# Performance work log

Measured on AMD Instinct MI355X. Metric: run time of the kernel, lower is better.

Reference implementation:

```python
import jax, jax.numpy as jnp
import numpy as np

N, M = 32768, 1024

def setup_inputs() -> dict:
    key = jax.random.key(0)
    k1, k2, k3, k4, k5 = jax.random.split(key, 5)
    origins = jax.random.normal(k1, (N, 2), dtype=jnp.float32)
    directions = jax.random.normal(k2, (N, 2), dtype=jnp.float32)
    means = jax.random.normal(k3, (M, 4), dtype=jnp.float32)
    # SPD covariances: A @ A^T + I so the inverse is well-defined
    A = jax.random.normal(k4, (M, 4, 4), dtype=jnp.float32) * 0.5
    covariances = jnp.einsum('mij,mkj->mik', A, A) + jnp.eye(4, dtype=jnp.float32)
    labels_embedding = jax.random.normal(k5, (M,), dtype=jnp.float32)
    return {"origins": origins, "directions": directions, "means": means,
            "covariances": covariances, "labels_embedding": labels_embedding}

def reference(origins, directions, means, covariances, labels_embedding):
    pos = jnp.concatenate([origins, directions], axis=1)          # [N,4]
    Sigma_inv = jnp.linalg.inv(covariances)                       # [M,4,4]
    diffs = pos[:, None, :] - means[None, :, :]                   # [N,M,4]
    quad = jnp.einsum('nmd,mde,nme->nm', diffs, Sigma_inv, diffs)  # [N,M]
    pdf = jnp.exp(-0.5 * quad) * labels_embedding[None, :]        # [N,M]
    prob = jax.nn.sigmoid(jnp.sum(pdf, axis=1))                   # [N]
    return prob.reshape(-1, 1)
```

## Files before the change

kernel.cpp:

```cpp
#include <hip/hip_runtime.h>
#include <math.h>

#define M_GAUSS 1024
#define N_RAYS  32768

typedef float v2f __attribute__((ext_vector_type(2)));

__device__ __forceinline__ float fexp2(float x) {
#if __has_builtin(__builtin_amdgcn_exp2f)
    return __builtin_amdgcn_exp2f(x);
#else
    return exp2f(x);
#endif
}

__device__ __forceinline__ v2f fma2(v2f a, v2f b, v2f c) {
#if __has_builtin(__builtin_elementwise_fma)
    return __builtin_elementwise_fma(a, b, c);
#else
    v2f r; r.x = fmaf(a.x, b.x, c.x); r.y = fmaf(a.y, b.y, c.y); return r;
#endif
}

__device__ __forceinline__ v2f mkv2(float x, float y) { v2f r; r.x = x; r.y = y; return r; }

__global__ __launch_bounds__(1024, 8) void decoder_fused(
    const float2* __restrict__ org,
    const float2* __restrict__ dir,
    const float*  __restrict__ means,
    const float*  __restrict__ covs,
    const float*  __restrict__ labels,
    float*        __restrict__ out)
{
    __shared__ float smemW[M_GAUSS * 16];

    const int tid  = threadIdx.x;
    const int lane = tid & 63;
    const int wave = tid >> 6;
    const int ray  = (blockIdx.x << 6) + lane;

    {
        const int g = tid;
        const float4* C4 = reinterpret_cast<const float4*>(covs + 16 * g);
        const float4 r0 = C4[0], r1 = C4[1], r2 = C4[2], r3 = C4[3];
        const float a00=r0.x, a01=r0.y, a02=r0.z, a03=r0.w;
        const float a10=r1.x, a11=r1.y, a12=r1.z, a13=r1.w;
        const float a20=r2.x, a21=r2.y, a22=r2.z, a23=r2.w;
        const float a30=r3.x, a31=r3.y, a32=r3.z, a33=r3.w;

        const float s0=a00*a11-a01*a10, s1=a00*a12-a02*a10, s2=a00*a13-a03*a10;
        const float s3=a01*a12-a02*a11, s4=a01*a13-a03*a11, s5=a02*a13-a03*a12;
        const float c5=a22*a33-a23*a32, c4=a21*a33-a23*a31, c3=a21*a32-a22*a31;
        const float c2=a20*a33-a23*a30, c1=a20*a32-a22*a30, c0=a20*a31-a21*a30;
        const float det = s0*c5 - s1*c4 + s2*c3 + s3*c2 - s4*c1 + s5*c0;
        const float id  = 1.0f / det;

        const float b00=( a11*c5 - a12*c4 + a13*c3)*id;
        const float b01=(-a01*c5 + a02*c4 - a03*c3)*id;
        const float b10=(-a10*c5 + a12*c2 - a13*c1)*id;
        const float b11=( a00*c5 - a02*c2 + a03*c1)*id;
        const float b20=( a10*c4 - a11*c2 + a13*c0)*id;
        const float b21=(-a00*c4 + a01*c2 - a03*c0)*id;
        const float b30=(-a10*c3 + a11*c1 - a12*c0)*id;
        const float b31=( a00*c3 - a01*c1 + a02*c0)*id;
        const float b02=( a31*s5 - a32*s4 + a33*s3)*id;
        const float b03=(-a21*s5 + a22*s4 - a23*s3)*id;
        const float b12=(-a30*s5 + a32*s2 - a33*s1)*id;
        const float b13=( a20*s5 - a22*s2 + a23*s1)*id;
        const float b22=( a30*s4 - a31*s2 + a33*s0)*id;
        const float b23=(-a20*s4 + a21*s2 - a23*s0)*id;
        const float b32=(-a30*s3 + a31*s1 - a32*s0)*id;
        const float b33=( a20*s3 - a21*s1 + a22*s0)*id;

        const float m01=0.5f*(b01+b10), m02=0.5f*(b02+b20), m03=0.5f*(b03+b30);
        const float m12=0.5f*(b12+b21), m13=0.5f*(b13+b31), m23=0.5f*(b23+b32);

        const float4 mu = reinterpret_cast<const float4*>(means)[g];
        const float u0=mu.x, u1=mu.y, u2=mu.z, u3=mu.w;
        const float v0 = b00*u0 + m01*u1 + m02*u2 + m03*u3;
        const float v1 = m01*u0 + b11*u1 + m12*u2 + m13*u3;
        const float v2 = m02*u0 + m12*u1 + b22*u2 + m23*u3;
        const float v3 = m03*u0 + m13*u1 + m23*u2 + b33*u3;
        const float cc = u0*v0 + u1*v1 + u2*v2 + u3*v3;

        const float k  = -0.72134752044448170368f;
        const float k2 = 2.0f * k;
        float* w = smemW + 16 * g;
        w[0]  = k*b00;   w[1]  = k*b11;   w[2]  = k*b22;   w[3]  = k*b33;
        w[4]  = k2*m01;  w[5]  = k2*m02;  w[6]  = k2*m03;  w[7]  = k2*m12;
        w[8]  = k2*m13;  w[9]  = k2*m23;  w[10] = -k2*v0;  w[11] = -k2*v1;
        w[12] = -k2*v2;  w[13] = -k2*v3;  w[14] = k*cc;    w[15] = labels[g];
    }
    __syncthreads();

    const float2 o = org[ray];
    const float2 d = dir[ray];
    const float p0=o.x, p1=o.y, p2=d.x, p3=d.y;

    const v2f f0 = mkv2(p0*p0, p1*p1);
    const v2f f1 = mkv2(p2*p2, p3*p3);
    const v2f f2 = mkv2(p0*p1, p0*p2);
    const v2f f3 = mkv2(p0*p3, p1*p2);
    const v2f f4 = mkv2(p1*p3, p2*p3);
    const v2f f5 = mkv2(p0, p1);
    const v2f f6 = mkv2(p2, p3);

    float acc = 0.0f;
    const int mBase = wave << 6;

    #pragma unroll 4
    for (int m = 0; m < 64; ++m) {
        const float4* w4 = reinterpret_cast<const float4*>(smemW + ((mBase + m) << 4));
        const float4 wa = w4[0];
        const float4 wb = w4[1];
        const float4 wc = w4[2];
        const float4 wd = w4[3];

        v2f cA = mkv2(wa.x, wa.y) * f0;
        v2f cB = mkv2(wa.z, wa.w) * f1;
        cA = fma2(mkv2(wb.x, wb.y), f2, cA);
        cB = fma2(mkv2(wb.z, wb.w), f3, cB);
        cA = fma2(mkv2(wc.x, wc.y), f4, cA);
        cB = fma2(mkv2(wc.z, wc.w), f5, cB);
        cA = fma2(mkv2(wd.x, wd.y), f6, cA);
        cA = cA + cB;
        const float s = (cA.x + cA.y) + wd.z;
        acc = fmaf(wd.w, fexp2(s), acc);
    }

    __syncthreads();
    smemW[(wave << 6) + lane] = acc;
    __syncthreads();

    if (wave == 0) {
        float t = 0.0f;
        #pragma unroll
        for (int w = 0; w < 16; ++w) t += smemW[(w << 6) + lane];
        const float e = fexp2(-t * 1.4426950408889634f);
        out[ray] = 1.0f / (1.0f + e);
    }
}

extern "C" void kernel_launch(void* const* d_in, const int* in_sizes, int n_in,
                              void* d_out, int out_size, void* d_ws, size_t ws_size,
                              hipStream_t stream) {
    const float* origins    = (const float*)d_in[0];
    const float* directions = (const float*)d_in[1];
    const float* means      = (const float*)d_in[2];
    const float* covs       = (const float*)d_in[3];
    const float* labels     = (const float*)d_in[4];
    float* out = (float*)d_out;

    decoder_fused<<<dim3(N_RAYS / 64), dim3(1024), 0, stream>>>(
        (const float2*)origins, (const float2*)directions, means, covs, labels, out);
}
```

Measured before the change: 80.76 us.

## Split covariance-inverse prep into a separate kernel and read weights from global memory

```diff
diff --git a/kernel.cpp b/kernel.cpp
--- a/kernel.cpp
+++ b/kernel.cpp
@@ -24,74 +24,76 @@
 
 __device__ __forceinline__ v2f mkv2(float x, float y) { v2f r; r.x = x; r.y = y; return r; }
 
-__global__ __launch_bounds__(1024, 8) void decoder_fused(
+__global__ __launch_bounds__(256) void prep_kernel(
+    const float* __restrict__ means,
+    const float* __restrict__ covs,
+    const float* __restrict__ labels,
+    float* __restrict__ W)
+{
+    const int g = blockIdx.x * blockDim.x + threadIdx.x;
+    if (g >= M_GAUSS) return;
+
+    const float4* C4 = reinterpret_cast<const float4*>(covs + 16 * g);
+    const float4 r0 = C4[0], r1 = C4[1], r2 = C4[2], r3 = C4[3];
+    const float a00=r0.x, a01=r0.y, a02=r0.z, a03=r0.w;
+    const float a10=r1.x, a11=r1.y, a12=r1.z, a13=r1.w;
+    const float a20=r2.x, a21=r2.y, a22=r2.z, a23=r2.w;
+    const float a30=r3.x, a31=r3.y, a32=r3.z, a33=r3.w;
+
+    const float s0=a00*a11-a01*a10, s1=a00*a12-a02*a10, s2=a00*a13-a03*a10;
+    const float s3=a01*a12-a02*a11, s4=a01*a13-a03*a11, s5=a02*a13-a03*a12;
+    const float c5=a22*a33-a23*a32, c4=a21*a33-a23*a31, c3=a21*a32-a22*a31;
+    const float c2=a20*a33-a23*a30, c1=a20*a32-a22*a30, c0=a20*a31-a21*a30;
+    const float det = s0*c5 - s1*c4 + s2*c3 + s3*c2 - s4*c1 + s5*c0;
+    const float id  = 1.0f / det;
+
+    const float b00=( a11*c5 - a12*c4 + a13*c3)*id;
+    const float b01=(-a01*c5 + a02*c4 - a03*c3)*id;
+    const float b10=(-a10*c5 + a12*c2 - a13*c1)*id;
+    const float b11=( a00*c5 - a02*c2 + a03*c1)*id;
+    const float b20=( a10*c4 - a11*c2 + a13*c0)*id;
+    const float b21=(-a00*c4 + a01*c2 - a03*c0)*id;
+    const float b30=(-a10*c3 + a11*c1 - a12*c0)*id;
+    const float b31=( a00*c3 - a01*c1 + a02*c0)*id;
+    const float b02=( a31*s5 - a32*s4 + a33*s3)*id;
+    const float b03=(-a21*s5 + a22*s4 - a23*s3)*id;
+    const float b12=(-a30*s5 + a32*s2 - a33*s1)*id;
+    const float b13=( a20*s5 - a22*s2 + a23*s1)*id;
+    const float b22=( a30*s4 - a31*s2 + a33*s0)*id;
+    const float b23=(-a20*s4 + a21*s2 - a23*s0)*id;
+    const float b32=(-a30*s3 + a31*s1 - a32*s0)*id;
+    const float b33=( a20*s3 - a21*s1 + a22*s0)*id;
+
+    const float m01=0.5f*(b01+b10), m02=0.5f*(b02+b20), m03=0.5f*(b03+b30);
+    const float m12=0.5f*(b12+b21), m13=0.5f*(b13+b31), m23=0.5f*(b23+b32);
+
+    const float4 mu = reinterpret_cast<const float4*>(means)[g];
+    const float u0=mu.x, u1=mu.y, u2=mu.z, u3=mu.w;
+    const float v0 = b00*u0 + m01*u1 + m02*u2 + m03*u3;
+    const float v1 = m01*u0 + b11*u1 + m12*u2 + m13*u3;
+    const float v2 = m02*u0 + m12*u1 + b22*u2 + m23*u3;
+    const float v3 = m03*u0 + m13*u1 + m23*u2 + b33*u3;
+    const float cc = u0*v0 + u1*v1 + u2*v2 + u3*v3;
+
+    const float k  = -0.72134752044448170368f;
+    const float k2 = 2.0f * k;
+    float4* w4 = reinterpret_cast<float4*>(W + 16 * g);
+    w4[0] = make_float4(k*b00,  k*b11,  k*b22,  k*b33);
+    w4[1] = make_float4(k2*m01, k2*m02, k2*m03, k2*m12);
+    w4[2] = make_float4(k2*m13, k2*m23, -k2*v0, -k2*v1);
+    w4[3] = make_float4(-k2*v2, -k2*v3, k*cc,   labels[g]);
+}
+
+__global__ __launch_bounds__(1024, 8) void decoder_kernel(
     const float2* __restrict__ org,
     const float2* __restrict__ dir,
-    const float*  __restrict__ means,
-    const float*  __restrict__ covs,
-    const float*  __restrict__ labels,
+    const float*  __restrict__ W,
     float*        __restrict__ out)
 {
-    __shared__ float smemW[M_GAUSS * 16];
-
     const int tid  = threadIdx.x;
     const int lane = tid & 63;
     const int wave = tid >> 6;
     const int ray  = (blockIdx.x << 6) + lane;
-
-    {
-        const int g = tid;
-        const float4* C4 = reinterpret_cast<const float4*>(covs + 16 * g);
-        const float4 r0 = C4[0], r1 = C4[1], r2 = C4[2], r3 = C4[3];
-        const float a00=r0.x, a01=r0.y, a02=r0.z, a03=r0.w;
-        const float a10=r1.x, a11=r1.y, a12=r1.z, a13=r1.w;
-        const float a20=r2.x, a21=r2.y, a22=r2.z, a23=r2.w;
-        const float a30=r3.x, a31=r3.y, a32=r3.z, a33=r3.w;
-
-        const float s0=a00*a11-a01*a10, s1=a00*a12-a02*a10, s2=a00*a13-a03*a10;
-        const float s3=a01*a12-a02*a11, s4=a01*a13-a03*a11, s5=a02*a13-a03*a12;
-        const float c5=a22*a33-a23*a32, c4=a21*a33-a23*a31, c3=a21*a32-a22*a31;
-        const float c2=a20*a33-a23*a30, c1=a20*a32-a22*a30, c0=a20*a31-a21*a30;
-        const float det = s0*c5 - s1*c4 + s2*c3 + s3*c2 - s4*c1 + s5*c0;
-        const float id  = 1.0f / det;
-
-        const float b00=( a11*c5 - a12*c4 + a13*c3)*id;
-        const float b01=(-a01*c5 + a02*c4 - a03*c3)*id;
-        const float b10=(-a10*c5 + a12*c2 - a13*c1)*id;
-        const float b11=( a00*c5 - a02*c2 + a03*c1)*id;
-        const float b20=( a10*c4 - a11*c2 + a13*c0)*id;
-        const float b21=(-a00*c4 + a01*c2 - a03*c0)*id;
-        const float b30=(-a10*c3 + a11*c1 - a12*c0)*id;
-        const float b31=( a00*c3 - a01*c1 + a02*c0)*id;
-        const float b02=( a31*s5 - a32*s4 + a33*s3)*id;
-        const float b03=(-a21*s5 + a22*s4 - a23*s3)*id;
-        const float b12=(-a30*s5 + a32*s2 - a33*s1)*id;
-        const float b13=( a20*s5 - a22*s2 + a23*s1)*id;
-        const float b22=( a30*s4 - a31*s2 + a33*s0)*id;
-        const float b23=(-a20*s4 + a21*s2 - a23*s0)*id;
-        const float b32=(-a30*s3 + a31*s1 - a32*s0)*id;
-        const float b33=( a20*s3 - a21*s1 + a22*s0)*id;
-
-        const float m01=0.5f*(b01+b10), m02=0.5f*(b02+b20), m03=0.5f*(b03+b30);
-        const float m12=0.5f*(b12+b21), m13=0.5f*(b13+b31), m23=0.5f*(b23+b32);
-
-        const float4 mu = reinterpret_cast<const float4*>(means)[g];
-        const float u0=mu.x, u1=mu.y, u2=mu.z, u3=mu.w;
-        const float v0 = b00*u0 + m01*u1 + m02*u2 + m03*u3;
-        const float v1 = m01*u0 + b11*u1 + m12*u2 + m13*u3;
-        const float v2 = m02*u0 + m12*u1 + b22*u2 + m23*u3;
-        const float v3 = m03*u0 + m13*u1 + m23*u2 + b33*u3;
-        const float cc = u0*v0 + u1*v1 + u2*v2 + u3*v3;
-
-        const float k  = -0.72134752044448170368f;
-        const float k2 = 2.0f * k;
-        float* w = smemW + 16 * g;
-        w[0]  = k*b00;   w[1]  = k*b11;   w[2]  = k*b22;   w[3]  = k*b33;
-        w[4]  = k2*m01;  w[5]  = k2*m02;  w[6]  = k2*m03;  w[7]  = k2*m12;
-        w[8]  = k2*m13;  w[9]  = k2*m23;  w[10] = -k2*v0;  w[11] = -k2*v1;
-        w[12] = -k2*v2;  w[13] = -k2*v3;  w[14] = k*cc;    w[15] = labels[g];
-    }
-    __syncthreads();
 
     const float2 o = org[ray];
     const float2 d = dir[ray];
@@ -105,12 +107,12 @@
     const v2f f5 = mkv2(p0, p1);
     const v2f f6 = mkv2(p2, p3);
 
+    const float* wptr = W + (__builtin_amdgcn_readfirstlane(wave << 6) << 4);
+
     float acc = 0.0f;
-    const int mBase = wave << 6;
-
     #pragma unroll 4
     for (int m = 0; m < 64; ++m) {
-        const float4* w4 = reinterpret_cast<const float4*>(smemW + ((mBase + m) << 4));
+        const float4* w4 = reinterpret_cast<const float4*>(wptr + (m << 4));
         const float4 wa = w4[0];
         const float4 wb = w4[1];
         const float4 wc = w4[2];
@@ -124,18 +126,17 @@
         cB = fma2(mkv2(wc.z, wc.w), f5, cB);
         cA = fma2(mkv2(wd.x, wd.y), f6, cA);
         cA = cA + cB;
-        const float s = (cA.x + cA.y) + wd.z;
-        acc = fmaf(wd.w, fexp2(s), acc);
+        acc = fmaf(wd.w, fexp2(cA.x + cA.y + wd.z), acc);
     }
 
-    __syncthreads();
-    smemW[(wave << 6) + lane] = acc;
+    __shared__ float partial[16][64];
+    partial[wave][lane] = acc;
     __syncthreads();
 
     if (wave == 0) {
         float t = 0.0f;
         #pragma unroll
-        for (int w = 0; w < 16; ++w) t += smemW[(w << 6) + lane];
+        for (int w = 0; w < 16; ++w) t += partial[w][lane];
         const float e = fexp2(-t * 1.4426950408889634f);
         out[ray] = 1.0f / (1.0f + e);
     }
@@ -150,7 +151,9 @@
     const float* covs       = (const float*)d_in[3];
     const float* labels     = (const float*)d_in[4];
     float* out = (float*)d_out;
+    float* W   = (float*)d_ws;
 
-    decoder_fused<<<dim3(N_RAYS / 64), dim3(1024), 0, stream>>>(
-        (const float2*)origins, (const float2*)directions, means, covs, labels, out);
+    prep_kernel<<<dim3(M_GAUSS / 256), dim3(256), 0, stream>>>(means, covs, labels, W);
+    decoder_kernel<<<dim3(N_RAYS / 64), dim3(1024), 0, stream>>>(
+        (const float2*)origins, (const float2*)directions, W, out);
 }
```

After: 78.05 us. 1.03x faster.

## Compute Gaussian quadratic forms via split-bf16 MFMA matmul in two-kernel pipeline

Applied to the files above, without the earlier changes.

```diff
diff --git a/kernel.cpp b/kernel.cpp
--- a/kernel.cpp
+++ b/kernel.cpp
@@ -1,10 +1,12 @@
 #include <hip/hip_runtime.h>
+#include <hip/hip_bf16.h>
 #include <math.h>
 
+#define N_RAYS  32768
 #define M_GAUSS 1024
-#define N_RAYS  32768
-
-typedef float v2f __attribute__((ext_vector_type(2)));
+
+typedef short v8s __attribute__((ext_vector_type(8)));
+typedef float v4f __attribute__((ext_vector_type(4)));
 
 __device__ __forceinline__ float fexp2(float x) {
 #if __has_builtin(__builtin_amdgcn_exp2f)
@@ -14,33 +16,55 @@
 #endif
 }
 
-__device__ __forceinline__ v2f fma2(v2f a, v2f b, v2f c) {
-#if __has_builtin(__builtin_elementwise_fma)
-    return __builtin_elementwise_fma(a, b, c);
-#else
-    v2f r; r.x = fmaf(a.x, b.x, c.x); r.y = fmaf(a.y, b.y, c.y); return r;
-#endif
-}
-
-__device__ __forceinline__ v2f mkv2(float x, float y) { v2f r; r.x = x; r.y = y; return r; }
-
-__global__ __launch_bounds__(1024, 8) void decoder_fused(
+union BFU { __hip_bfloat16 b; unsigned short u; };
+__device__ __forceinline__ unsigned short f2bf(float f) { BFU x; x.b = __float2bfloat16(f); return x.u; }
+__device__ __forceinline__ float bf2f(unsigned short u)  { BFU x; x.u = u; return __bfloat162float(x.b); }
+
+__device__ __forceinline__ void split_bf16(float f, unsigned short& hi, unsigned short& lo) {
+    hi = f2bf(f);
+    lo = f2bf(f - bf2f(hi));
+}
+
+__device__ __forceinline__ void store8(unsigned short* dst, const unsigned short* s) {
+    uint4 v;
+    v.x = (unsigned)s[0] | ((unsigned)s[1] << 16);
+    v.y = (unsigned)s[2] | ((unsigned)s[3] << 16);
+    v.z = (unsigned)s[4] | ((unsigned)s[5] << 16);
+    v.w = (unsigned)s[6] | ((unsigned)s[7] << 16);
+    *reinterpret_cast<uint4*>(dst) = v;
+}
+
+__global__ __launch_bounds__(256) void prep_kernel(
     const float2* __restrict__ org,
     const float2* __restrict__ dir,
     const float*  __restrict__ means,
     const float*  __restrict__ covs,
-    const float*  __restrict__ labels,
-    float*        __restrict__ out)
+    unsigned short* __restrict__ Fs,
+    unsigned short* __restrict__ Bt)
 {
-    __shared__ float smemW[M_GAUSS * 16];
-
-    const int tid  = threadIdx.x;
-    const int lane = tid & 63;
-    const int wave = tid >> 6;
-    const int ray  = (blockIdx.x << 6) + lane;
+    const int n = blockIdx.x * 256 + threadIdx.x;
 
     {
-        const int g = tid;
+        const float2 o = org[n];
+        const float2 d = dir[n];
+        const float p0 = o.x, p1 = o.y, p2 = d.x, p3 = d.y;
+        float f[16] = { p0*p0, p1*p1, p2*p2, p3*p3,
+                        p0*p1, p0*p2, p0*p3, p1*p2, p1*p3, p2*p3,
+                        p0, p1, p2, p3, 1.0f, 0.0f };
+        unsigned short hi[16], lo[16];
+        #pragma unroll
+        for (int k = 0; k < 16; ++k) split_bf16(f[k], hi[k], lo[k]);
+
+        const int rt = n >> 4, c = n & 15;
+        unsigned short* base = Fs + (size_t)rt * 64 * 8;
+        store8(base + (0*16 + c) * 8, hi + 0);
+        store8(base + (1*16 + c) * 8, hi + 8);
+        store8(base + (2*16 + c) * 8, lo + 0);
+        store8(base + (3*16 + c) * 8, lo + 8);
+    }
+
+    if (n < M_GAUSS) {
+        const int g = n;
         const float4* C4 = reinterpret_cast<const float4*>(covs + 16 * g);
         const float4 r0 = C4[0], r1 = C4[1], r2 = C4[2], r3 = C4[3];
         const float a00=r0.x, a01=r0.y, a02=r0.z, a03=r0.w;
@@ -85,59 +109,96 @@
 
         const float k  = -0.72134752044448170368f;
         const float k2 = 2.0f * k;
-        float* w = smemW + 16 * g;
-        w[0]  = k*b00;   w[1]  = k*b11;   w[2]  = k*b22;   w[3]  = k*b33;
-        w[4]  = k2*m01;  w[5]  = k2*m02;  w[6]  = k2*m03;  w[7]  = k2*m12;
-        w[8]  = k2*m13;  w[9]  = k2*m23;  w[10] = -k2*v0;  w[11] = -k2*v1;
-        w[12] = -k2*v2;  w[13] = -k2*v3;  w[14] = k*cc;    w[15] = labels[g];
-    }
-    __syncthreads();
-
-    const float2 o = org[ray];
-    const float2 d = dir[ray];
-    const float p0=o.x, p1=o.y, p2=d.x, p3=d.y;
-
-    const v2f f0 = mkv2(p0*p0, p1*p1);
-    const v2f f1 = mkv2(p2*p2, p3*p3);
-    const v2f f2 = mkv2(p0*p1, p0*p2);
-    const v2f f3 = mkv2(p0*p3, p1*p2);
-    const v2f f4 = mkv2(p1*p3, p2*p3);
-    const v2f f5 = mkv2(p0, p1);
-    const v2f f6 = mkv2(p2, p3);
-
-    float acc = 0.0f;
-    const int mBase = wave << 6;
-
-    #pragma unroll 4
-    for (int m = 0; m < 64; ++m) {
-        const float4* w4 = reinterpret_cast<const float4*>(smemW + ((mBase + m) << 4));
-        const float4 wa = w4[0];
-        const float4 wb = w4[1];
-        const float4 wc = w4[2];
-        const float4 wd = w4[3];
-
-        v2f cA = mkv2(wa.x, wa.y) * f0;
-        v2f cB = mkv2(wa.z, wa.w) * f1;
-        cA = fma2(mkv2(wb.x, wb.y), f2, cA);
-        cB = fma2(mkv2(wb.z, wb.w), f3, cB);
-        cA = fma2(mkv2(wc.x, wc.y), f4, cA);
-        cB = fma2(mkv2(wc.z, wc.w), f5, cB);
-        cA = fma2(mkv2(wd.x, wd.y), f6, cA);
-        cA = cA + cB;
-        const float s = (cA.x + cA.y) + wd.z;
-        acc = fmaf(wd.w, fexp2(s), acc);
-    }
-
-    __syncthreads();
-    smemW[(wave << 6) + lane] = acc;
-    __syncthreads();
-
-    if (wave == 0) {
-        float t = 0.0f;
-        #pragma unroll
-        for (int w = 0; w < 16; ++w) t += smemW[(w << 6) + lane];
-        const float e = fexp2(-t * 1.4426950408889634f);
-        out[ray] = 1.0f / (1.0f + e);
+        float w[16] = { k*b00,  k*b11,  k*b22,  k*b33,
+                        k2*m01, k2*m02, k2*m03, k2*m12, k2*m13, k2*m23,
+                        -k2*v0, -k2*v1, -k2*v2, -k2*v3, k*cc, 0.0f };
+        unsigned short whi[16], wlo[16];
+        #pragma unroll
+        for (int q = 0; q < 16; ++q) split_bf16(w[q], whi[q], wlo[q]);
+
+        const int t = g >> 4, cg = g & 15;
+        unsigned short* b1 = Bt + (size_t)t * 32 * 8;
+        store8(b1 + (0*16 + cg) * 8, whi + 0);
+        store8(b1 + (1*16 + cg) * 8, whi + 8);
+        unsigned short* b2 = Bt + (size_t)2048 * 8 + (size_t)t * 32 * 8;
+        store8(b2 + (0*16 + cg) * 8, wlo + 0);
+        store8(b2 + (1*16 + cg) * 8, wlo + 8);
+    }
+}
+
+__global__ __launch_bounds__(512) void decoder_kernel(
+    const uint4* __restrict__ Fs,
+    const uint4* __restrict__ Btg,
+    const float* __restrict__ labels,
+    float*       __restrict__ out)
+{
+    __shared__ uint4 lds[4096];
+
+    const int tid = threadIdx.x;
+    const int L   = tid & 63;
+    const int w   = tid >> 6;
+    const int c15 = L & 15;
+    const int q   = L >> 4;
+
+    #pragma unroll
+    for (int i = 0; i < 8; ++i) lds[i * 512 + tid] = Btg[i * 512 + tid];
+
+    const int rt0 = blockIdx.x * 4;
+    v8s af[4];
+    #pragma unroll
+    for (int rt = 0; rt < 4; ++rt) {
+        union { uint4 u; v8s s; } x;
+        x.u = Fs[(size_t)(rt0 + rt) * 64 + L];
+        af[rt] = x.s;
+    }
+    __syncthreads();
+
+    v4f acc[4];
+    #pragma unroll
+    for (int rt = 0; rt < 4; ++rt) acc[rt] = (v4f){0.f, 0.f, 0.f, 0.f};
+
+    const bool loHalf = (L < 32);
+    #pragma unroll 2
+    for (int i = 0; i < 8; ++i) {
+        const int t = w * 8 + i;
+        union { uint4 u; v8s s; } b1x, b2x;
+        b1x.u = lds[t * 32 + (L & 31)];
+        uint4 b2u = lds[2048 + t * 32 + (L & 31)];
+        if (!loHalf) { b2u.x = 0; b2u.y = 0; b2u.z = 0; b2u.w = 0; }
+        b2x.u = b2u;
+        const float lab = labels[t * 16 + c15];
+
+        #pragma unroll
+        for (int rt = 0; rt < 4; ++rt) {
+            v4f cz = (v4f){0.f, 0.f, 0.f, 0.f};
+            v4f s = __builtin_amdgcn_mfma_f32_16x16x32_bf16(af[rt], b2x.s, cz, 0, 0, 0);
+            s = __builtin_amdgcn_mfma_f32_16x16x32_bf16(af[rt], b1x.s, s, 0, 0, 0);
+            #pragma unroll
+            for (int r = 0; r < 4; ++r)
+                acc[rt][r] = fmaf(lab, fexp2(s[r]), acc[rt][r]);
+        }
+    }
+
+    __syncthreads();
+    float* P = reinterpret_cast<float*>(lds);
+    for (int i = tid; i < 64 * 17; i += 512) P[i] = 0.f;
+    __syncthreads();
+    #pragma unroll
+    for (int rt = 0; rt < 4; ++rt) {
+        #pragma unroll
+        for (int r = 0; r < 4; ++r) {
+            const int ray = rt * 16 + q * 4 + r;
+            atomicAdd(&P[ray * 17 + c15], acc[rt][r]);
+        }
+    }
+    __syncthreads();
+
+    if (tid < 64) {
+        float tsum = 0.f;
+        #pragma unroll
+        for (int c = 0; c < 16; ++c) tsum += P[tid * 17 + c];
+        const float e = fexp2(-tsum * 1.4426950408889634f);
+        out[blockIdx.x * 64 + tid] = 1.0f / (1.0f + e);
     }
 }
 
@@ -151,6 +212,12 @@
     const float* labels     = (const float*)d_in[4];
     float* out = (float*)d_out;
 
-    decoder_fused<<<dim3(N_RAYS / 64), dim3(1024), 0, stream>>>(
-        (const float2*)origins, (const float2*)directions, means, covs, labels, out);
-}
+    char* ws = (char*)d_ws;
+    unsigned short* Fs = (unsigned short*)ws;
+    unsigned short* Bt = (unsigned short*)(ws + (size_t)2 * 1024 * 1024);
+
+    prep_kernel<<<dim3(N_RAYS / 256), dim3(256), 0, stream>>>(
+        (const float2*)origins, (const float2*)directions, means, covs, Fs, Bt);
+    decoder_kernel<<<dim3(N_RAYS / 64), dim3(512), 0, stream>>>(
+        (const uint4*)Fs, (const uint4*)Bt, labels, out);
+}
```

Result: slower. 89.26 us (+10.5%).
